# Kernel tuning notes

Hardware: AMD Instinct MI355X
Metric: run time of the kernel (lower is better)

Reference implementation:

```python
import jax, jax.numpy as jnp
import numpy as np

D_MODEL = 1024
NUM_HEADS = 16
HEAD_DIM = D_MODEL // NUM_HEADS  # 64


def setup_inputs() -> dict:
    key = jax.random.key(0)
    k1, k2, k3 = jax.random.split(key, 3)
    x = jax.random.normal(k1, (4, 2048, D_MODEL), dtype=jnp.float32)
    w_qkv = jax.random.normal(k2, (3 * D_MODEL, D_MODEL), dtype=jnp.float32) * 0.02
    b_qkv = jnp.zeros((3 * D_MODEL,), dtype=jnp.float32)
    w_out = jax.random.normal(k3, (D_MODEL, D_MODEL), dtype=jnp.float32) * 0.02
    b_out = jnp.zeros((D_MODEL,), dtype=jnp.float32)
    return {"x": x, "w_qkv": w_qkv, "b_qkv": b_qkv, "w_out": w_out, "b_out": b_out}


def reference(x, w_qkv, b_qkv, w_out, b_out):
    N, S, _ = x.shape
    # qkv projection: (N, S, 3*D) -> (3, N, heads, S, head_dim), matching torch permute(2,0,3,1,4)
    qkv = (jnp.einsum('nsd,ed->nse', x, w_qkv) + b_qkv)
    qkv = qkv.reshape(N, S, 3, NUM_HEADS, HEAD_DIM).transpose(2, 0, 3, 1, 4)
    queries, keys, values = qkv[0], qkv[1], qkv[2]  # each (N, heads, S, head_dim)
    # Faithful to source: einsum labels axis1 as 'q'/'k' and axis2 as 'h',
    # so energy has shape (N, S, heads, heads) -- attention over the heads axis.
    energy = jnp.einsum('nqhd,nkhd->nhqk', queries, keys)
    attention = jax.nn.softmax(energy / jnp.sqrt(jnp.float32(HEAD_DIM)), axis=3)
    out = jnp.einsum('nhql,nlhd->nqhd', attention, values).reshape(N, S, D_MODEL)
    return jnp.einsum('nsd,od->nso', out, w_out) + b_out
```

## Files before the change

### kernel.cpp

```cpp
#include <hip/hip_runtime.h>
#include <hip/hip_bf16.h>


typedef __hip_bfloat16 bf16;
using bf16x8 = __attribute__((ext_vector_type(8))) short;
using f32x4  = __attribute__((ext_vector_type(4))) float;

__device__ __forceinline__ float b2f(unsigned short u) {
    return __uint_as_float(((unsigned)u) << 16);
}
__device__ __forceinline__ unsigned short f2b(float f) {
    bf16 h = __float2bfloat16(f);
    return *reinterpret_cast<unsigned short*>(&h);
}
__device__ __forceinline__ void store1(float* p, float v) { *p = v; }
__device__ __forceinline__ void store1(bf16* p, float v) { *p = __float2bfloat16(v); }

__device__ __forceinline__ void gload_lds16(const bf16* g, bf16* l) {
    __builtin_amdgcn_global_load_lds(
        (const __attribute__((address_space(1))) void*)g,
        (__attribute__((address_space(3))) void*)l, 16, 0, 0);
}

#define BAR()  __builtin_amdgcn_s_barrier()
#define LGK()  asm volatile("s_waitcnt lgkmcnt(0)" ::: "memory")
#define VMC(N) asm volatile("s_waitcnt vmcnt(" #N ")" ::: "memory")

template <typename CT>
__global__ __launch_bounds__(512, 2)
void gemm3b(const bf16* __restrict__ A, const bf16* __restrict__ B,
            const float* __restrict__ bias, CT* __restrict__ C,
            int M, int N, int K, int gx) {
    __shared__ alignas(1024) bf16 smem[3][384 * 64];

    const int t    = threadIdx.x;
    const int lane = t & 63;
    const int wid  = t >> 6;
    const int wr   = wid >> 2;
    const int wc   = wid & 3;

    const int nwg = gridDim.x;
    const int bid = blockIdx.x;
    const int wg  = (bid & 7) * (nwg >> 3) + (bid >> 3);
    const int m0  = (wg / gx) * 128;
    const int n0  = (wg % gx) * 256;

    const int nt = K / 64;

    const int srow = lane >> 3;
    const int kel  = ((lane & 7) ^ (lane >> 3)) * 8;

    auto stageA = [&](int tt) {
        if (tt >= nt) return;
        bf16* lp = &smem[tt % 3][wid * 1024];
        const bf16* gp = A + (size_t)(m0 + wid * 16 + srow) * K + tt * 64 + kel;
        gload_lds16(gp, lp);
        gload_lds16(gp + (size_t)8 * K, lp + 512);
    };
    auto stageB = [&](int tt, int h) {
        if (tt >= nt) return;
        bf16* lp = &smem[tt % 3][8192 + h * 8192 + wid * 1024];
        const bf16* gp = B + (size_t)(n0 + h * 128 + wid * 16 + srow) * K + tt * 64 + kel;
        gload_lds16(gp, lp);
        gload_lds16(gp + (size_t)8 * K, lp + 512);
    };

    const int arow_base = wr * 64 + (lane & 15);
    const int brow_base = wc * 64 + (lane & 15);
    const int kqb       = (lane >> 4) * 16;
    auto LDA = [&](int buf, int kk, int m) -> bf16x8 {
        const int row = arow_base + m * 16;
        const int ab  = row * 128 + ((kk * 64 + kqb) ^ ((row & 7) << 4));
        return *(const bf16x8*)((const char*)&smem[buf][0] + ab);
    };
    auto LDB = [&](int buf, int kk, int n) -> bf16x8 {
        const int row = brow_base + n * 16;
        const int bb  = 16384 + row * 128 + ((kk * 64 + kqb) ^ ((row & 7) << 4));
        return *(const bf16x8*)((const char*)&smem[buf][0] + bb);
    };

    f32x4 acc[4][4] = {};
    bf16x8 af[4], bfr[4];

    stageA(0); stageB(0, 0); stageB(0, 1);
    stageA(1); stageB(1, 0); stageB(1, 1);
    VMC(6);
    BAR();

    for (int tt = 0; tt < nt; ++tt) {
        const int buf = tt % 3;

#pragma unroll
        for (int m = 0; m < 4; ++m) af[m] = LDA(buf, 0, m);
#pragma unroll
        for (int n = 0; n < 4; ++n) bfr[n] = LDB(buf, 0, n);
        stageA(tt + 2);
        BAR(); LGK();
        __builtin_amdgcn_s_setprio(1);
#pragma unroll
        for (int m = 0; m < 4; ++m)
#pragma unroll
            for (int n = 0; n < 4; ++n)
                acc[m][n] = __builtin_amdgcn_mfma_f32_16x16x32_bf16(
                    af[m], bfr[n], acc[m][n], 0, 0, 0);
        __builtin_amdgcn_s_setprio(0);
        BAR();

#pragma unroll
        for (int m = 0; m < 4; ++m) af[m] = LDA(buf, 1, m);
#pragma unroll
        for (int n = 0; n < 4; ++n) bfr[n] = LDB(buf, 1, n);
        stageB(tt + 2, 0); stageB(tt + 2, 1);
        if (tt < nt - 2) { VMC(6); } else { VMC(0); }
        BAR(); LGK();
        __builtin_amdgcn_s_setprio(1);
#pragma unroll
        for (int m = 0; m < 4; ++m)
#pragma unroll
            for (int n = 0; n < 4; ++n)
                acc[m][n] = __builtin_amdgcn_mfma_f32_16x16x32_bf16(
                    af[m], bfr[n], acc[m][n], 0, 0, 0);
        __builtin_amdgcn_s_setprio(0);
        BAR();
    }

#pragma unroll
    for (int m = 0; m < 4; ++m) {
        const int row = m0 + wr * 64 + m * 16 + (lane >> 4) * 4;
#pragma unroll
        for (int n = 0; n < 4; ++n) {
            const int col = n0 + wc * 64 + n * 16 + (lane & 15);
            const float bval = bias[col];
#pragma unroll
            for (int r = 0; r < 4; ++r)
                store1(&C[(size_t)(row + r) * N + col], acc[m][n][r] + bval);
        }
    }
}

__global__ __launch_bounds__(256)
void cvt_f32_bf16(const float* __restrict__ in, bf16* __restrict__ out, int n4) {
    int i = blockIdx.x * 256 + threadIdx.x;
    if (i >= n4) return;
    float4 v = ((const float4*)in)[i];
    ushort4 o = {f2b(v.x), f2b(v.y), f2b(v.z), f2b(v.w)};
    ((ushort4*)out)[i] = o;
}

__global__ __launch_bounds__(256)
void attn_kernel(const bf16* __restrict__ qkv, bf16* __restrict__ T) {
    __shared__ float lds[4][48 * 68];

    const int wave = threadIdx.x >> 6;
    const int lane = threadIdx.x & 63;
    const int token = blockIdx.x * 4 + wave;
    const int n = token >> 11;
    const int s = token & 2047;

    float* L = lds[wave];
    const bf16* src = qkv + (size_t)token * 3072;

#pragma unroll
    for (int i = 0; i < 6; ++i) {
        int idx = i * 64 + lane;
        uint4 v = *reinterpret_cast<const uint4*>(src + (size_t)idx * 8);
        int e0 = idx * 8;
        float* dst = &L[(e0 >> 6) * 68 + (e0 & 63)];
        float4 a, b;
        a.x = b2f((unsigned short)(v.x & 0xffff));
        a.y = b2f((unsigned short)(v.x >> 16));
        a.z = b2f((unsigned short)(v.y & 0xffff));
        a.w = b2f((unsigned short)(v.y >> 16));
        b.x = b2f((unsigned short)(v.z & 0xffff));
        b.y = b2f((unsigned short)(v.z >> 16));
        b.z = b2f((unsigned short)(v.w & 0xffff));
        b.w = b2f((unsigned short)(v.w >> 16));
        *(float4*)dst = a;
        *(float4*)(dst + 4) = b;
    }
    __syncthreads();

    const int q0 = lane & 15;
    const int g  = lane >> 4;

    float e[4] = {0.f, 0.f, 0.f, 0.f};
    const float* Qr = &L[q0 * 68];
    const float* K0 = &L[(16 + g * 4) * 68];
#pragma unroll
    for (int d = 0; d < 64; d += 4) {
        float4 q4 = *(const float4*)(Qr + d);
#pragma unroll
        for (int j = 0; j < 4; ++j) {
            float4 k4 = *(const float4*)(K0 + j * 68 + d);
            e[j] += q4.x * k4.x + q4.y * k4.y + q4.z * k4.z + q4.w * k4.w;
        }
    }
#pragma unroll
    for (int j = 0; j < 4; ++j) e[j] *= 0.125f;

    float m = fmaxf(fmaxf(e[0], e[1]), fmaxf(e[2], e[3]));
    m = fmaxf(m, __shfl_xor(m, 16));
    m = fmaxf(m, __shfl_xor(m, 32));
    float p[4], sum = 0.f;
#pragma unroll
    for (int j = 0; j < 4; ++j) { p[j] = __expf(e[j] - m); sum += p[j]; }
    sum += __shfl_xor(sum, 16);
    sum += __shfl_xor(sum, 32);
    const float inv = 1.0f / sum;

    float prow[16];
#pragma unroll
    for (int j = 0; j < 4; ++j) {
        prow[g * 4 + j]         = p[j] * inv;
        prow[((g ^ 1) * 4) + j] = __shfl_xor(p[j], 16) * inv;
        prow[((g ^ 2) * 4) + j] = __shfl_xor(p[j], 32) * inv;
        prow[((g ^ 3) * 4) + j] = __shfl_xor(p[j], 48) * inv;
    }

    const int d0 = g * 16;
    float4 o4[4] = {};
#pragma unroll
    for (int k = 0; k < 16; ++k) {
        const float p1 = prow[k];
        const float* Vr = &L[(32 + k) * 68 + d0];
#pragma unroll
        for (int c = 0; c < 4; ++c) {
            float4 v = *(const float4*)(Vr + c * 4);
            o4[c].x += p1 * v.x; o4[c].y += p1 * v.y;
            o4[c].z += p1 * v.z; o4[c].w += p1 * v.w;
        }
    }
    unsigned short outv[16];
#pragma unroll
    for (int c = 0; c < 4; ++c) {
        outv[c * 4 + 0] = f2b(o4[c].x); outv[c * 4 + 1] = f2b(o4[c].y);
        outv[c * 4 + 2] = f2b(o4[c].z); outv[c * 4 + 3] = f2b(o4[c].w);
    }
    const int sp = q0 * 128 + (s >> 4);
    size_t off = ((size_t)n * 2048 + sp) * 1024 + (size_t)(s & 15) * 64 + d0;
    uint4* dst = reinterpret_cast<uint4*>(T + off);
    const uint4* sv = reinterpret_cast<const uint4*>(outv);
    dst[0] = sv[0];
    dst[1] = sv[1];
}

extern "C" void kernel_launch(void* const* d_in, const int* in_sizes, int n_in,
                              void* d_out, int out_size, void* d_ws, size_t ws_size,
                              hipStream_t stream) {
    const float* x     = (const float*)d_in[0];
    const float* w_qkv = (const float*)d_in[1];
    const float* b_qkv = (const float*)d_in[2];
    const float* w_out = (const float*)d_in[3];
    const float* b_out = (const float*)d_in[4];
    float* out = (float*)d_out;

    const int M = 8192, E = 3072, K = 1024, D = 1024;

    bf16* qkv = (bf16*)d_ws;
    bf16* T   = qkv + (size_t)M * E;
    bf16* W2b = qkv;
    bf16* W1b = (bf16*)d_out;
    bf16* X16 = W1b + (size_t)E * K;

    dim3 blk(256);

    cvt_f32_bf16<<<dim3(M * K / 4 / 256), blk, 0, stream>>>(x, X16, M * K / 4);
    cvt_f32_bf16<<<dim3(E * K / 4 / 256), blk, 0, stream>>>(w_qkv, W1b, E * K / 4);
    gemm3b<bf16><<<dim3((M / 128) * (E / 256)), dim3(512), 0, stream>>>(
        X16, W1b, b_qkv, qkv, M, E, K, E / 256);
    attn_kernel<<<dim3(M / 4), blk, 0, stream>>>(qkv, T);
    cvt_f32_bf16<<<dim3(D * K / 4 / 256), blk, 0, stream>>>(w_out, W2b, D * K / 4);
    gemm3b<float><<<dim3((M / 128) * (D / 256)), dim3(512), 0, stream>>>(
        T, W2b, b_out, out, M, D, K, D / 256);
}
```

Before: 130.1 us.

## Software-pipeline LDS fragment loads with MFMA using double-buffered registers

```diff
diff --git a/kernel.cpp b/kernel.cpp
--- a/kernel.cpp
+++ b/kernel.cpp
@@ -22,13 +22,13 @@
         (__attribute__((address_space(3))) void*)l, 16, 0, 0);
 }
 
-#define BAR()  __builtin_amdgcn_s_barrier()
-#define LGK()  asm volatile("s_waitcnt lgkmcnt(0)" ::: "memory")
-#define VMC(N) asm volatile("s_waitcnt vmcnt(" #N ")" ::: "memory")
+#define BAR()   __builtin_amdgcn_s_barrier()
+#define LGKM(N) asm volatile("s_waitcnt lgkmcnt(" #N ")" ::: "memory")
+#define VMC(N)  asm volatile("s_waitcnt vmcnt(" #N ")" ::: "memory")
 
 template <typename CT>
 __global__ __launch_bounds__(512, 2)
-void gemm3b(const bf16* __restrict__ A, const bf16* __restrict__ B,
+void gemm3p(const bf16* __restrict__ A, const bf16* __restrict__ B,
             const float* __restrict__ bias, CT* __restrict__ C,
             int M, int N, int K, int gx) {
     __shared__ alignas(1024) bf16 smem[3][384 * 64];
@@ -80,46 +80,54 @@
     };
 
     f32x4 acc[4][4] = {};
-    bf16x8 af[4], bfr[4];
+    bf16x8 afc[4], bfc[4];
+    bf16x8 afa[4], bfa[4];
 
     stageA(0); stageB(0, 0); stageB(0, 1);
     stageA(1); stageB(1, 0); stageB(1, 1);
     VMC(6);
     BAR();
+#pragma unroll
+    for (int m = 0; m < 4; ++m) afc[m] = LDA(0, 0, m);
+#pragma unroll
+    for (int n = 0; n < 4; ++n) bfc[n] = LDB(0, 0, n);
 
     for (int tt = 0; tt < nt; ++tt) {
         const int buf = tt % 3;
 
 #pragma unroll
-        for (int m = 0; m < 4; ++m) af[m] = LDA(buf, 0, m);
-#pragma unroll
-        for (int n = 0; n < 4; ++n) bfr[n] = LDB(buf, 0, n);
-        stageA(tt + 2);
-        BAR(); LGK();
+        for (int m = 0; m < 4; ++m) afa[m] = LDA(buf, 1, m);
+#pragma unroll
+        for (int n = 0; n < 4; ++n) bfa[n] = LDB(buf, 1, n);
+        stageA(tt + 2); stageB(tt + 2, 0); stageB(tt + 2, 1);
+        LGKM(8);
         __builtin_amdgcn_s_setprio(1);
 #pragma unroll
         for (int m = 0; m < 4; ++m)
 #pragma unroll
             for (int n = 0; n < 4; ++n)
                 acc[m][n] = __builtin_amdgcn_mfma_f32_16x16x32_bf16(
-                    af[m], bfr[n], acc[m][n], 0, 0, 0);
+                    afc[m], bfc[n], acc[m][n], 0, 0, 0);
         __builtin_amdgcn_s_setprio(0);
+        if (tt < nt - 2) { VMC(6); } else { VMC(0); }
         BAR();
-
-#pragma unroll
-        for (int m = 0; m < 4; ++m) af[m] = LDA(buf, 1, m);
-#pragma unroll
-        for (int n = 0; n < 4; ++n) bfr[n] = LDB(buf, 1, n);
-        stageB(tt + 2, 0); stageB(tt + 2, 1);
-        if (tt < nt - 2) { VMC(6); } else { VMC(0); }
-        BAR(); LGK();
+        if (tt + 1 < nt) {
+            const int nb = (tt + 1) % 3;
+#pragma unroll
+            for (int m = 0; m < 4; ++m) afc[m] = LDA(nb, 0, m);
+#pragma unroll
+            for (int n = 0; n < 4; ++n) bfc[n] = LDB(nb, 0, n);
+            LGKM(8);
+        } else {
+            LGKM(0);
+        }
         __builtin_amdgcn_s_setprio(1);
 #pragma unroll
         for (int m = 0; m < 4; ++m)
 #pragma unroll
             for (int n = 0; n < 4; ++n)
                 acc[m][n] = __builtin_amdgcn_mfma_f32_16x16x32_bf16(
-                    af[m], bfr[n], acc[m][n], 0, 0, 0);
+                    afa[m], bfa[n], acc[m][n], 0, 0, 0);
         __builtin_amdgcn_s_setprio(0);
         BAR();
     }
@@ -266,10 +274,10 @@
 
     cvt_f32_bf16<<<dim3(M * K / 4 / 256), blk, 0, stream>>>(x, X16, M * K / 4);
     cvt_f32_bf16<<<dim3(E * K / 4 / 256), blk, 0, stream>>>(w_qkv, W1b, E * K / 4);
-    gemm3b<bf16><<<dim3((M / 128) * (E / 256)), dim3(512), 0, stream>>>(
+    gemm3p<bf16><<<dim3((M / 128) * (E / 256)), dim3(512), 0, stream>>>(
         X16, W1b, b_qkv, qkv, M, E, K, E / 256);
     attn_kernel<<<dim3(M / 4), blk, 0, stream>>>(qkv, T);
     cvt_f32_bf16<<<dim3(D * K / 4 / 256), blk, 0, stream>>>(w_out, W2b, D * K / 4);
-    gemm3b<float><<<dim3((M / 128) * (D / 256)), dim3(512), 0, stream>>>(
+    gemm3p<float><<<dim3((M / 128) * (D / 256)), dim3(512), 0, stream>>>(
         T, W2b, b_out, out, M, D, K, D / 256);
 }
```

New measurement: 127.9 us. No clear change (-1.6%).
